# Performance work log

Measured on AMD Instinct MI355X. Metric: run time of the kernel, lower is better.

The kernel has to match this reference:

```python
import jax, jax.numpy as jnp
import numpy as np

N_NODES = 50000


def gcn_conv(x, edge_index, W, b, num_nodes):
    """PyG GCNConv: add self-loops, symmetric norm, gather-scatter aggregate."""
    h = x @ W  # [N, out]
    row = jnp.concatenate([edge_index[0], jnp.arange(num_nodes)])  # sources (+ self loops)
    col = jnp.concatenate([edge_index[1], jnp.arange(num_nodes)])  # targets
    deg = jax.ops.segment_sum(jnp.ones_like(col, dtype=h.dtype), col, num_segments=num_nodes)
    dinv = jnp.where(deg > 0, jax.lax.rsqrt(deg), 0.0)
    norm = dinv[row] * dinv[col]  # [E+N]
    msgs = h[row] * norm[:, None]  # gather + scale
    out = jax.ops.segment_sum(msgs, col, num_segments=num_nodes)  # scatter-add
    return out + b


def setup_inputs() -> dict:
    key = jax.random.key(0)
    ks = jax.random.split(key, 8)
    F_in, H, D = 50, 50, 64
    E_train, Ep, En = 1600000, 200000, 200000
    x = jax.random.normal(ks[0], (N_NODES, F_in), dtype=jnp.float32)
    train_pos_edge_index = jax.random.randint(ks[1], (2, E_train), 0, N_NODES)
    pos_edge_index = jax.random.randint(ks[2], (2, Ep), 0, N_NODES)
    neg_edge_index = jax.random.randint(ks[3], (2, En), 0, N_NODES)
    # Glorot-ish params for the two GCN layers
    W1 = jax.random.normal(ks[4], (F_in, H), dtype=jnp.float32) * (1.0 / np.sqrt(F_in))
    b1 = jnp.zeros((H,), dtype=jnp.float32)
    W2 = jax.random.normal(ks[5], (H, D), dtype=jnp.float32) * (1.0 / np.sqrt(H))
    b2 = jnp.zeros((D,), dtype=jnp.float32)
    return {"x": x, "train_pos_edge_index": train_pos_edge_index,
            "pos_edge_index": pos_edge_index, "neg_edge_index": neg_edge_index,
            "W1": W1, "b1": b1, "W2": W2, "b2": b2}


def reference(x, train_pos_edge_index, pos_edge_index, neg_edge_index, W1, b1, W2, b2):
    # encode: conv1 -> relu -> conv2
    h = gcn_conv(x, train_pos_edge_index, W1, b1, N_NODES)
    h = jax.nn.relu(h)
    z = gcn_conv(h, train_pos_edge_index, W2, b2, N_NODES)  # [N, D]
    # decode: dot product over concatenated pos/neg edge endpoints
    edge_index = jnp.concatenate([pos_edge_index, neg_edge_index], axis=-1)
    logits = jnp.sum(z[edge_index[0]] * z[edge_index[1]], axis=-1)  # [Ep+En]
    return logits
```

## Files before the change

### kernel.cpp

```cpp
#include <hip/hip_runtime.h>
#include <hip/hip_bf16.h>
#include <hip/hip_fp16.h>


constexpr int N_NODES = 50000;
constexpr int NBITS = 6;
constexpr int BNODES = 1 << NBITS;
constexpr int NBUCK = (N_NODES + BNODES - 1) / BNODES;
constexpr int CAP = 2560;
constexpr int CHUNK = 6144;
constexpr int PTHREADS = 512;
constexpr int CTHREADS = 512;
constexpr int NTILE = 8;
constexpr int TROWS = 6250;

union H4 {
    uint2 u;
    __half2 h[2];
};

union H8 {
    uint4 u;
    __half2 h[4];
};

__device__ inline H4 f4_to_h4(float4 v) {
    H4 r;
    r.h[0] = __floats2half2_rn(v.x, v.y);
    r.h[1] = __floats2half2_rn(v.z, v.w);
    return r;
}

__device__ inline uint4 pack8(float4 A, float4 B) {
    H8 r;
    r.h[0] = __floats2half2_rn(A.x, A.y);
    r.h[1] = __floats2half2_rn(A.z, A.w);
    r.h[2] = __floats2half2_rn(B.x, B.y);
    r.h[3] = __floats2half2_rn(B.z, B.w);
    return r.u;
}

__device__ inline void unpack8(uint4 w, int* r) {
    r[0] = (int)(w.x & 0xffffu);  r[1] = (int)(w.x >> 16);
    r[2] = (int)(w.y & 0xffffu);  r[3] = (int)(w.y >> 16);
    r[4] = (int)(w.z & 0xffffu);  r[5] = (int)(w.z >> 16);
    r[6] = (int)(w.w & 0xffffu);  r[7] = (int)(w.w >> 16);
}

__device__ inline void add8(float4& A, float4& B, H8 v) {
    float2 g0 = __half22float2(v.h[0]);
    float2 g1 = __half22float2(v.h[1]);
    float2 g2 = __half22float2(v.h[2]);
    float2 g3 = __half22float2(v.h[3]);
    A.x += g0.x; A.y += g0.y; A.z += g1.x; A.w += g1.y;
    B.x += g2.x; B.y += g2.y; B.z += g3.x; B.w += g3.y;
}

__device__ inline void fma8(float4& A, float4& B, H8 v, float m) {
    float2 g0 = __half22float2(v.h[0]);
    float2 g1 = __half22float2(v.h[1]);
    float2 g2 = __half22float2(v.h[2]);
    float2 g3 = __half22float2(v.h[3]);
    A.x = fmaf(m, g0.x, A.x); A.y = fmaf(m, g0.y, A.y);
    A.z = fmaf(m, g1.x, A.z); A.w = fmaf(m, g1.y, A.w);
    B.x = fmaf(m, g2.x, B.x); B.y = fmaf(m, g2.y, B.y);
    B.z = fmaf(m, g3.x, B.z); B.w = fmaf(m, g3.y, B.w);
}

__device__ inline float hdot2(unsigned ua, unsigned ub) {
    __half2 ha = *(__half2*)&ua;
    __half2 hb = *(__half2*)&ub;
    float2 fa = __half22float2(ha);
    float2 fb = __half22float2(hb);
    return fa.x * fb.x + fa.y * fb.y;
}

__global__ __launch_bounds__(PTHREADS) void partition_kernel(const int4* __restrict__ row4,
                                                             const int4* __restrict__ col4, int E,
                                                             int* __restrict__ cursor,
                                                             unsigned* __restrict__ bEdges) {
    __shared__ unsigned ed2[CHUNK];
    __shared__ unsigned char tick[CHUNK];
    __shared__ int cnt[NBUCK];
    __shared__ int loff[NBUCK];
    __shared__ int base[NBUCK];
    int t = threadIdx.x;
    int e0 = blockIdx.x * CHUNK;
    int n = min(CHUNK, E - e0);
    int n4 = n >> 2;
    for (int i = t; i < NBUCK; i += PTHREADS) cnt[i] = 0;
    __syncthreads();
    const int4* r4 = row4 + (e0 >> 2);
    const int4* c4 = col4 + (e0 >> 2);
    for (int i = t; i < n4; i += PTHREADS) {
        int4 c = c4[i];
        tick[i * 4 + 0] = (unsigned char)atomicAdd(&cnt[c.x >> NBITS], 1);
        tick[i * 4 + 1] = (unsigned char)atomicAdd(&cnt[c.y >> NBITS], 1);
        tick[i * 4 + 2] = (unsigned char)atomicAdd(&cnt[c.z >> NBITS], 1);
        tick[i * 4 + 3] = (unsigned char)atomicAdd(&cnt[c.w >> NBITS], 1);
    }
    __syncthreads();
    if (t < 64) {
        constexpr int SEG = (NBUCK + 63) / 64;
        int lo = t * SEG;
        int hi = min(lo + SEG, NBUCK);
        int s = 0;
        for (int i = lo; i < hi; ++i) {
            loff[i] = s;
            s += cnt[i];
        }
        int tot = s;
        int ex = tot;
#pragma unroll
        for (int off = 1; off < 64; off <<= 1) {
            int o = __shfl_up(ex, off, 64);
            if (t >= off) ex += o;
        }
        ex -= tot;
        for (int i = lo; i < hi; ++i) loff[i] += ex;
    }
    __syncthreads();
    for (int i = t; i < NBUCK; i += PTHREADS) base[i] = cnt[i] ? atomicAdd(&cursor[i], cnt[i]) : 0;
    for (int i = t; i < n4; i += PTHREADS) {
        int4 r = r4[i];
        int4 c = c4[i];
        unsigned p0 = ((unsigned)r.x << 16) | (unsigned)c.x;
        unsigned p1 = ((unsigned)r.y << 16) | (unsigned)c.y;
        unsigned p2 = ((unsigned)r.z << 16) | (unsigned)c.z;
        unsigned p3 = ((unsigned)r.w << 16) | (unsigned)c.w;
        ed2[loff[c.x >> NBITS] + (int)tick[i * 4 + 0]] = p0;
        ed2[loff[c.y >> NBITS] + (int)tick[i * 4 + 1]] = p1;
        ed2[loff[c.z >> NBITS] + (int)tick[i * 4 + 2]] = p2;
        ed2[loff[c.w >> NBITS] + (int)tick[i * 4 + 3]] = p3;
    }
    __syncthreads();
    for (int s = t; s < n; s += PTHREADS) {
        unsigned p = ed2[s];
        int bk = (int)(p & 0xffffu) >> NBITS;
        int pos = base[bk] + (s - loff[bk]);
        if (pos < CAP) bEdges[(size_t)bk * CAP + pos] = p;
    }
}

__global__ __launch_bounds__(CTHREADS) void bucket_csr_mm_kernel(const int* __restrict__ cursor,
                                                                 const unsigned* __restrict__ bEdges,
                                                                 const float* __restrict__ x,
                                                                 const float* __restrict__ W1,
                                                                 unsigned short* __restrict__ srcIdx,
                                                                 unsigned* __restrict__ rowmeta,
                                                                 float* __restrict__ dinv,
                                                                 uint2* __restrict__ Hs, int N) {
    __shared__ alignas(16) unsigned ed[CAP];
    __shared__ alignas(16) unsigned short srcL[CAP];
    __shared__ unsigned char tick[CAP];
    __shared__ int tdeg[BNODES * NTILE];
    __shared__ int toff[BNODES * NTILE];
    __shared__ int totPad;
    __shared__ float dinvL[BNODES];
    __shared__ float4 Ws4[50 * 16];
    __shared__ float xs[BNODES][51];
    int b = blockIdx.x;
    int tx = threadIdx.x;
    int cnt = min(cursor[b], CAP);
    for (int i = tx; i < BNODES * NTILE; i += CTHREADS) tdeg[i] = 0;
    {
        uint4* z4 = (uint4*)srcL;
        uint4 z = make_uint4(0u, 0u, 0u, 0u);
        for (int i = tx; i < (CAP >> 3); i += CTHREADS) z4[i] = z;
    }
    __syncthreads();
    const uint4* s4 = (const uint4*)(bEdges + (size_t)b * CAP);
    int cnt4 = cnt >> 2;
    for (int i = tx; i < cnt4; i += CTHREADS) {
        uint4 w = s4[i];
        ((uint4*)ed)[i] = w;
        unsigned pp[4] = {w.x, w.y, w.z, w.w};
#pragma unroll
        for (int u = 0; u < 4; ++u) {
            unsigned p = pp[u];
            int l = (int)(p & (BNODES - 1));
            int tl = (int)(p >> 16) / TROWS;
            tick[i * 4 + u] = (unsigned char)atomicAdd(&tdeg[l * NTILE + tl], 1);
        }
    }
    for (int i = cnt4 * 4 + tx; i < cnt; i += CTHREADS) {
        unsigned p = bEdges[(size_t)b * CAP + i];
        ed[i] = p;
        int l = (int)(p & (BNODES - 1));
        int tl = (int)(p >> 16) / TROWS;
        tick[i] = (unsigned char)atomicAdd(&tdeg[l * NTILE + tl], 1);
    }
    for (int i = tx; i < 50 * 64; i += CTHREADS) {
        int k = i >> 6;
        int c = i & 63;
        ((float*)Ws4)[i] = (c < 50) ? W1[k * 50 + c] : 0.f;
    }
    for (int i = tx; i < BNODES * 50; i += CTHREADS) {
        int l = i / 50;
        int k = i - l * 50;
        int node = b * BNODES + l;
        xs[l][k] = (node < N) ? x[(size_t)node * 50 + k] : 0.f;
    }
    __syncthreads();
    if (tx < BNODES) {
        int sd[NTILE];
        int d = 0;
#pragma unroll
        for (int u = 0; u < NTILE; ++u) {
            sd[u] = tdeg[tx * NTILE + u];
            d += sd[u];
        }
        int dpad = (d + 7) & ~7;
        int s = dpad;
#pragma unroll
        for (int off = 1; off < BNODES; off <<= 1) {
            int o = __shfl_up(s, off, 64);
            if (tx >= off) s += o;
        }
        int ex = s - dpad;
        int run = ex;
#pragma unroll
        for (int u = 0; u < NTILE; ++u) {
            toff[tx * NTILE + u] = run;
            run += sd[u];
        }
        if (tx == 63) totPad = min(s, CAP);
        float dvv = rsqrtf((float)d + 1.0f);
        dinvL[tx] = dvv;
        int node = b * BNODES + tx;
        if (node < N) {
            unsigned st = (unsigned)(b * CAP + ex);
            rowmeta[node] = (st << 7) | (unsigned)d;
            dinv[node] = dvv;
        }
    }
    __syncthreads();
    for (int i = tx; i < cnt; i += CTHREADS) {
        unsigned p = ed[i];
        int l = (int)(p & (BNODES - 1));
        int tl = (int)(p >> 16) / TROWS;
        int pos = toff[l * NTILE + tl] + (int)tick[i];
        if (pos < CAP) srcL[pos] = (unsigned short)(p >> 16);
    }
    __syncthreads();
    int tot = totPad;
    {
        const uint4* sl4 = (const uint4*)srcL;
        uint4* si4 = (uint4*)(srcIdx + (size_t)b * CAP);
        for (int i = tx; i < (tot >> 3); i += CTHREADS) si4[i] = sl4[i];
    }
    int q = tx & 15;
    int g = tx >> 4;
#pragma unroll
    for (int rep = 0; rep < 2; ++rep) {
        int l = g + rep * 32;
        float4 acc = make_float4(0.f, 0.f, 0.f, 0.f);
#pragma unroll
        for (int k = 0; k < 50; ++k) {
            float xv = xs[l][k];
            float4 w = Ws4[k * 16 + q];
            acc.x = fmaf(xv, w.x, acc.x);
            acc.y = fmaf(xv, w.y, acc.y);
            acc.z = fmaf(xv, w.z, acc.z);
            acc.w = fmaf(xv, w.w, acc.w);
        }
        float dv = dinvL[l];
        acc.x *= dv;
        acc.y *= dv;
        acc.z *= dv;
        acc.w *= dv;
        int node = b * BNODES + l;
        if (node < N) Hs[(size_t)node * 16 + q] = f4_to_h4(acc).u;
    }
}

__device__ inline void gather_sum8(const unsigned short* __restrict__ srcIdx,
                                   const uint4* __restrict__ hs, int node, int q,
                                   unsigned meta, float4& A, float4& B) {
    int start = (int)(meta >> 7);
    int d = (int)(meta & 127u);
    int end = start + d;
    H8 t;
    t.u = hs[(size_t)node * 8 + q];
    {
        float2 g0 = __half22float2(t.h[0]);
        float2 g1 = __half22float2(t.h[1]);
        float2 g2 = __half22float2(t.h[2]);
        float2 g3 = __half22float2(t.h[3]);
        A = make_float4(g0.x, g0.y, g1.x, g1.y);
        B = make_float4(g2.x, g2.y, g3.x, g3.y);
    }
    if (d == 0) return;
    int j = start;
    uint4 w = *(const uint4*)(srcIdx + j);
    while (j + 8 <= end) {
        uint4 wc = w;
        if (j + 8 < end) w = *(const uint4*)(srcIdx + j + 8);
        int r[8];
        unpack8(wc, r);
#pragma unroll
        for (int u = 0; u < 8; ++u) {
            H8 hv;
            hv.u = hs[(size_t)r[u] * 8 + q];
            add8(A, B, hv);
        }
        j += 8;
    }
    if (j < end) {
        int r[8];
        unpack8(w, r);
#pragma unroll
        for (int u = 0; u < 8; ++u) {
            float m = (j + u < end) ? 1.f : 0.f;
            H8 hv;
            hv.u = hs[(size_t)r[u] * 8 + q];
            fma8(A, B, hv, m);
        }
    }
}

template <int BC>
__global__ __launch_bounds__(256) void agg_mm_kernel(const unsigned* __restrict__ rowmeta,
                                                     const unsigned short* __restrict__ srcIdx,
                                                     const uint4* __restrict__ hs,
                                                     const float* __restrict__ dinv,
                                                     const float* __restrict__ b1,
                                                     const float* __restrict__ W2,
                                                     uint4* __restrict__ out, int N) {
    __shared__ float4 Ws4[50 * 16];
    __shared__ float h1s[32][68];
    for (int i = threadIdx.x; i < 50 * 64; i += 256) ((float*)Ws4)[i] = W2[i];
    int tid = blockIdx.x * blockDim.x + threadIdx.x;
    int node = tid >> 3;
    int q = tid & 7;
    int g = threadIdx.x >> 3;
    int nodeC = min(node, N - 1);
    float4 A = make_float4(0.f, 0.f, 0.f, 0.f), B = A;
    if (q < 7) gather_sum8(srcIdx, hs, nodeC, q, rowmeta[nodeC], A, B);
    float dv = dinv[nodeC];
    int f = q * 8;
    float hv[8] = {A.x, A.y, A.z, A.w, B.x, B.y, B.z, B.w};
#pragma unroll
    for (int u = 0; u < 8; ++u) {
        float bb = (f + u < BC) ? b1[f + u] : 0.f;
        h1s[g][f + u] = fmaxf(dv * hv[u] + bb, 0.f);
    }
    __syncthreads();
    float4 aA = make_float4(0.f, 0.f, 0.f, 0.f), aB = aA;
#pragma unroll
    for (int k = 0; k < 50; ++k) {
        float xv = h1s[g][k];
        float4 wA = Ws4[k * 16 + 2 * q];
        float4 wB = Ws4[k * 16 + 2 * q + 1];
        aA.x = fmaf(xv, wA.x, aA.x);
        aA.y = fmaf(xv, wA.y, aA.y);
        aA.z = fmaf(xv, wA.z, aA.z);
        aA.w = fmaf(xv, wA.w, aA.w);
        aB.x = fmaf(xv, wB.x, aB.x);
        aB.y = fmaf(xv, wB.y, aB.y);
        aB.z = fmaf(xv, wB.z, aB.z);
        aB.w = fmaf(xv, wB.w, aB.w);
    }
    aA.x *= dv; aA.y *= dv; aA.z *= dv; aA.w *= dv;
    aB.x *= dv; aB.y *= dv; aB.z *= dv; aB.w *= dv;
    if (node < N) out[(size_t)node * 8 + q] = pack8(aA, aB);
}

template <int BC>
__global__ __launch_bounds__(256) void agg_kernel(const unsigned* __restrict__ rowmeta,
                                                  const unsigned short* __restrict__ srcIdx,
                                                  const uint4* __restrict__ hs,
                                                  const float* __restrict__ dinv,
                                                  const float* __restrict__ b,
                                                  uint4* __restrict__ out, int N) {
    int tid = blockIdx.x * blockDim.x + threadIdx.x;
    int node = tid >> 3;
    int q = tid & 7;
    if (node >= N) return;
    float4 A, B;
    gather_sum8(srcIdx, hs, node, q, rowmeta[node], A, B);
    float dv = dinv[node];
    int f = q * 8;
    float hv[8] = {A.x, A.y, A.z, A.w, B.x, B.y, B.z, B.w};
    float o[8];
#pragma unroll
    for (int u = 0; u < 8; ++u) o[u] = dv * hv[u] + (f + u < BC ? b[f + u] : 0.f);
    out[(size_t)node * 8 + q] =
        pack8(make_float4(o[0], o[1], o[2], o[3]), make_float4(o[4], o[5], o[6], o[7]));
}

__global__ __launch_bounds__(256) void decode_kernel(const int* __restrict__ pos,
                                                     const int* __restrict__ neg, int Ep, int En,
                                                     const uint4* __restrict__ z4,
                                                     float* __restrict__ logits) {
    int tid = blockIdx.x * blockDim.x + threadIdx.x;
    int e = tid >> 3;
    int q = tid & 7;
    int Etot = Ep + En;
    if (e >= Etot) return;
    int a, bn;
    if (e < Ep) {
        a = pos[e];
        bn = pos[Ep + e];
    } else {
        int t = e - Ep;
        a = neg[t];
        bn = neg[En + t];
    }
    uint4 ua = z4[(size_t)a * 8 + q];
    uint4 ub = z4[(size_t)bn * 8 + q];
    float v = hdot2(ua.x, ub.x) + hdot2(ua.y, ub.y) + hdot2(ua.z, ub.z) + hdot2(ua.w, ub.w);
    v += __shfl_xor(v, 1, 64);
    v += __shfl_xor(v, 2, 64);
    v += __shfl_xor(v, 4, 64);
    if (q == 0) logits[e] = v;
}

extern "C" void kernel_launch(void* const* d_in, const int* in_sizes, int n_in,
                              void* d_out, int out_size, void* d_ws, size_t ws_size,
                              hipStream_t stream) {
    const float* x = (const float*)d_in[0];
    const int* train = (const int*)d_in[1];
    const int* pos = (const int*)d_in[2];
    const int* neg = (const int*)d_in[3];
    const float* W1 = (const float*)d_in[4];
    const float* b1 = (const float*)d_in[5];
    const float* W2 = (const float*)d_in[6];
    const float* b2 = (const float*)d_in[7];
    float* logits = (float*)d_out;

    const int FIN = 50;
    const int N = in_sizes[0] / FIN;
    const int E = in_sizes[1] / 2;
    const int Ep = in_sizes[2] / 2;
    const int En = in_sizes[3] / 2;

    const int* t_row = train;
    const int* t_col = train + E;

    float* dinv = (float*)d_ws;
    __half* buf0 = (__half*)(dinv + N);
    __half* buf1 = buf0 + (size_t)N * 64;
    unsigned* rowmeta = (unsigned*)(buf1 + (size_t)N * 64);
    int* cursor = (int*)(rowmeta + N);
    uintptr_t sp = (uintptr_t)(cursor + NBUCK);
    sp = (sp + 15) & ~(uintptr_t)15;
    unsigned short* srcIdx = (unsigned short*)sp;
    uintptr_t bp = (uintptr_t)(srcIdx + (size_t)NBUCK * CAP);
    bp = (bp + 15) & ~(uintptr_t)15;
    unsigned* bEdges = (unsigned*)bp;

    hipMemsetAsync(cursor, 0, (size_t)NBUCK * sizeof(int), stream);

    partition_kernel<<<(E + CHUNK - 1) / CHUNK, PTHREADS, 0, stream>>>((const int4*)t_row,
                                                                       (const int4*)t_col, E,
                                                                       cursor, bEdges);
    bucket_csr_mm_kernel<<<NBUCK, CTHREADS, 0, stream>>>(cursor, bEdges, x, W1, srcIdx, rowmeta,
                                                         dinv, (uint2*)buf0, N);

    const int AGB = (N * 8 + 255) / 256;

    agg_mm_kernel<50><<<AGB, 256, 0, stream>>>(rowmeta, srcIdx, (const uint4*)buf0, dinv, b1, W2,
                                               (uint4*)buf1, N);
    agg_kernel<64><<<AGB, 256, 0, stream>>>(rowmeta, srcIdx, (const uint4*)buf1, dinv, b2,
                                            (uint4*)buf0, N);
    decode_kernel<<<((Ep + En) * 8 + 255) / 256, 256, 0, stream>>>(pos, neg, Ep, En,
                                                                   (const uint4*)buf0, logits);
}
```

Baseline: 197.5 us.

## Split each aggregation into two source-range phases with fp32 partial sums

Each GCN aggregation is split into two passes. The first gathers neighbours whose source index lies in the lower half of the node range and writes fp32 partial sums. The second gathers the upper half, adds the partials, and applies the epilogue. The aim is to keep the half of the feature table each pass touches resident in cache, and nontemporal loads and stores are added for streamed data to reduce cache pollution. In exchange there are two extra kernel launches and a 12.8MB partial-sum buffer written and read back per layer.

```diff
diff --git a/kernel.cpp b/kernel.cpp
--- a/kernel.cpp
+++ b/kernel.cpp
@@ -13,6 +13,30 @@
 constexpr int CTHREADS = 512;
 constexpr int NTILE = 8;
 constexpr int TROWS = 6250;
+constexpr int SPLIT_ROW = 4 * TROWS;
+
+typedef unsigned int u32x4 __attribute__((ext_vector_type(4)));
+typedef float f32x4 __attribute__((ext_vector_type(4)));
+
+__device__ inline uint4 ntload_u4(const uint4* p) {
+    u32x4 v = __builtin_nontemporal_load((const u32x4*)p);
+    return make_uint4(v.x, v.y, v.z, v.w);
+}
+
+__device__ inline void ntstore_u4(uint4* p, uint4 v) {
+    u32x4 t = {v.x, v.y, v.z, v.w};
+    __builtin_nontemporal_store(t, (u32x4*)p);
+}
+
+__device__ inline float4 ntload_f4(const float4* p) {
+    f32x4 v = __builtin_nontemporal_load((const f32x4*)p);
+    return make_float4(v.x, v.y, v.z, v.w);
+}
+
+__device__ inline void ntstore_f4(float4* p, float4 v) {
+    f32x4 t = {v.x, v.y, v.z, v.w};
+    __builtin_nontemporal_store(t, (f32x4*)p);
+}
 
 union H4 {
     uint2 u;
@@ -148,6 +172,7 @@
                                                                  const float* __restrict__ W1,
                                                                  unsigned short* __restrict__ srcIdx,
                                                                  unsigned* __restrict__ rowmeta,
+                                                                 unsigned char* __restrict__ dlo,
                                                                  float* __restrict__ dinv,
                                                                  uint2* __restrict__ Hs, int N) {
     __shared__ alignas(16) unsigned ed[CAP];
@@ -210,6 +235,7 @@
             sd[u] = tdeg[tx * NTILE + u];
             d += sd[u];
         }
+        int dl = sd[0] + sd[1] + sd[2] + sd[3];
         int dpad = (d + 7) & ~7;
         int s = dpad;
 #pragma unroll
@@ -231,6 +257,7 @@
         if (node < N) {
             unsigned st = (unsigned)(b * CAP + ex);
             rowmeta[node] = (st << 7) | (unsigned)d;
+            dlo[node] = (unsigned char)dl;
             dinv[node] = dvv;
         }
     }
@@ -274,30 +301,28 @@
     }
 }
 
-__device__ inline void gather_sum8(const unsigned short* __restrict__ srcIdx,
-                                   const uint4* __restrict__ hs, int node, int q,
-                                   unsigned meta, float4& A, float4& B) {
-    int start = (int)(meta >> 7);
-    int d = (int)(meta & 127u);
-    int end = start + d;
-    H8 t;
-    t.u = hs[(size_t)node * 8 + q];
-    {
-        float2 g0 = __half22float2(t.h[0]);
-        float2 g1 = __half22float2(t.h[1]);
-        float2 g2 = __half22float2(t.h[2]);
-        float2 g3 = __half22float2(t.h[3]);
-        A = make_float4(g0.x, g0.y, g1.x, g1.y);
-        B = make_float4(g2.x, g2.y, g3.x, g3.y);
-    }
-    if (d == 0) return;
-    int j = start;
-    uint4 w = *(const uint4*)(srcIdx + j);
-    while (j + 8 <= end) {
-        uint4 wc = w;
-        if (j + 8 < end) w = *(const uint4*)(srcIdx + j + 8);
+__device__ inline void gather_range8(const unsigned short* __restrict__ srcIdx,
+                                     const uint4* __restrict__ hs, int jlo, int jhi,
+                                     int q, float4& A, float4& B) {
+    if (jlo >= jhi) return;
+    int j = jlo & ~7;
+    if (j < jlo) {
+        uint4 w = ntload_u4((const uint4*)(srcIdx + j));
         int r[8];
-        unpack8(wc, r);
+        unpack8(w, r);
+#pragma unroll
+        for (int u = 0; u < 8; ++u) {
+            bool ok = (j + u >= jlo) && (j + u < jhi);
+            H8 hv;
+            hv.u = hs[(size_t)(ok ? r[u] : 0) * 8 + q];
+            fma8(A, B, hv, ok ? 1.f : 0.f);
+        }
+        j += 8;
+    }
+    while (j + 8 <= jhi) {
+        uint4 w = ntload_u4((const uint4*)(srcIdx + j));
+        int r[8];
+        unpack8(w, r);
 #pragma unroll
         for (int u = 0; u < 8; ++u) {
             H8 hv;
@@ -306,27 +331,54 @@
         }
         j += 8;
     }
-    if (j < end) {
+    if (j < jhi) {
+        uint4 w = ntload_u4((const uint4*)(srcIdx + j));
         int r[8];
         unpack8(w, r);
 #pragma unroll
         for (int u = 0; u < 8; ++u) {
-            float m = (j + u < end) ? 1.f : 0.f;
+            bool ok = (j + u < jhi);
             H8 hv;
-            hv.u = hs[(size_t)r[u] * 8 + q];
-            fma8(A, B, hv, m);
-        }
-    }
+            hv.u = hs[(size_t)(ok ? r[u] : 0) * 8 + q];
+            fma8(A, B, hv, ok ? 1.f : 0.f);
+        }
+    }
+}
+
+template <int QMAX>
+__global__ __launch_bounds__(256) void agg_phaseA_kernel(const unsigned* __restrict__ rowmeta,
+                                                         const unsigned char* __restrict__ dlo,
+                                                         const unsigned short* __restrict__ srcIdx,
+                                                         const uint4* __restrict__ hs,
+                                                         float4* __restrict__ part, int N) {
+    int tid = blockIdx.x * blockDim.x + threadIdx.x;
+    int node = tid >> 3;
+    int q = tid & 7;
+    if (node >= N || q >= QMAX) return;
+    unsigned meta = rowmeta[node];
+    int start = (int)(meta >> 7);
+    int jmid = start + (int)dlo[node];
+    float4 A = make_float4(0.f, 0.f, 0.f, 0.f), B = A;
+    if (node < SPLIT_ROW) {
+        H8 s;
+        s.u = hs[(size_t)node * 8 + q];
+        add8(A, B, s);
+    }
+    gather_range8(srcIdx, hs, start, jmid, q, A, B);
+    ntstore_f4(&part[(size_t)node * 16 + 2 * q], A);
+    ntstore_f4(&part[(size_t)node * 16 + 2 * q + 1], B);
 }
 
 template <int BC>
-__global__ __launch_bounds__(256) void agg_mm_kernel(const unsigned* __restrict__ rowmeta,
-                                                     const unsigned short* __restrict__ srcIdx,
-                                                     const uint4* __restrict__ hs,
-                                                     const float* __restrict__ dinv,
-                                                     const float* __restrict__ b1,
-                                                     const float* __restrict__ W2,
-                                                     uint4* __restrict__ out, int N) {
+__global__ __launch_bounds__(256) void agg_mm_phaseB_kernel(const unsigned* __restrict__ rowmeta,
+                                                            const unsigned char* __restrict__ dlo,
+                                                            const unsigned short* __restrict__ srcIdx,
+                                                            const uint4* __restrict__ hs,
+                                                            const float4* __restrict__ part,
+                                                            const float* __restrict__ dinv,
+                                                            const float* __restrict__ b1,
+                                                            const float* __restrict__ W2,
+                                                            uint4* __restrict__ out, int N) {
     __shared__ float4 Ws4[50 * 16];
     __shared__ float h1s[32][68];
     for (int i = threadIdx.x; i < 50 * 64; i += 256) ((float*)Ws4)[i] = W2[i];
@@ -335,8 +387,21 @@
     int q = tid & 7;
     int g = threadIdx.x >> 3;
     int nodeC = min(node, N - 1);
+    unsigned meta = rowmeta[nodeC];
+    int start = (int)(meta >> 7);
+    int d = (int)(meta & 127u);
+    int jmid = start + (int)dlo[nodeC];
     float4 A = make_float4(0.f, 0.f, 0.f, 0.f), B = A;
-    if (q < 7) gather_sum8(srcIdx, hs, nodeC, q, rowmeta[nodeC], A, B);
+    if (q < 7) {
+        A = ntload_f4(&part[(size_t)nodeC * 16 + 2 * q]);
+        B = ntload_f4(&part[(size_t)nodeC * 16 + 2 * q + 1]);
+        if (nodeC >= SPLIT_ROW) {
+            H8 s;
+            s.u = hs[(size_t)nodeC * 8 + q];
+            add8(A, B, s);
+        }
+        gather_range8(srcIdx, hs, jmid, start + d, q, A, B);
+    }
     float dv = dinv[nodeC];
     int f = q * 8;
     float hv[8] = {A.x, A.y, A.z, A.w, B.x, B.y, B.z, B.w};
@@ -363,30 +428,42 @@
     }
     aA.x *= dv; aA.y *= dv; aA.z *= dv; aA.w *= dv;
     aB.x *= dv; aB.y *= dv; aB.z *= dv; aB.w *= dv;
-    if (node < N) out[(size_t)node * 8 + q] = pack8(aA, aB);
+    if (node < N) ntstore_u4(&out[(size_t)node * 8 + q], pack8(aA, aB));
 }
 
 template <int BC>
-__global__ __launch_bounds__(256) void agg_kernel(const unsigned* __restrict__ rowmeta,
-                                                  const unsigned short* __restrict__ srcIdx,
-                                                  const uint4* __restrict__ hs,
-                                                  const float* __restrict__ dinv,
-                                                  const float* __restrict__ b,
-                                                  uint4* __restrict__ out, int N) {
+__global__ __launch_bounds__(256) void agg_phaseB_kernel(const unsigned* __restrict__ rowmeta,
+                                                         const unsigned char* __restrict__ dlo,
+                                                         const unsigned short* __restrict__ srcIdx,
+                                                         const uint4* __restrict__ hs,
+                                                         const float4* __restrict__ part,
+                                                         const float* __restrict__ dinv,
+                                                         const float* __restrict__ b,
+                                                         uint4* __restrict__ out, int N) {
     int tid = blockIdx.x * blockDim.x + threadIdx.x;
     int node = tid >> 3;
     int q = tid & 7;
     if (node >= N) return;
-    float4 A, B;
-    gather_sum8(srcIdx, hs, node, q, rowmeta[node], A, B);
+    unsigned meta = rowmeta[node];
+    int start = (int)(meta >> 7);
+    int d = (int)(meta & 127u);
+    int jmid = start + (int)dlo[node];
+    float4 A = ntload_f4(&part[(size_t)node * 16 + 2 * q]);
+    float4 B = ntload_f4(&part[(size_t)node * 16 + 2 * q + 1]);
+    if (node >= SPLIT_ROW) {
+        H8 s;
+        s.u = hs[(size_t)node * 8 + q];
+        add8(A, B, s);
+    }
+    gather_range8(srcIdx, hs, jmid, start + d, q, A, B);
     float dv = dinv[node];
     int f = q * 8;
     float hv[8] = {A.x, A.y, A.z, A.w, B.x, B.y, B.z, B.w};
     float o[8];
 #pragma unroll
     for (int u = 0; u < 8; ++u) o[u] = dv * hv[u] + (f + u < BC ? b[f + u] : 0.f);
-    out[(size_t)node * 8 + q] =
-        pack8(make_float4(o[0], o[1], o[2], o[3]), make_float4(o[4], o[5], o[6], o[7]));
+    ntstore_u4(&out[(size_t)node * 8 + q],
+               pack8(make_float4(o[0], o[1], o[2], o[3]), make_float4(o[4], o[5], o[6], o[7])));
 }
 
 __global__ __launch_bounds__(256) void decode_kernel(const int* __restrict__ pos,
@@ -449,21 +526,29 @@
     uintptr_t bp = (uintptr_t)(srcIdx + (size_t)NBUCK * CAP);
     bp = (bp + 15) & ~(uintptr_t)15;
     unsigned* bEdges = (unsigned*)bp;
-
-    hipMemsetAsync(cursor, 0, (size_t)NBUCK * sizeof(int), stream);
+    unsigned char* dlo = (unsigned char*)(bEdges + (size_t)NBUCK * CAP);
+    uintptr_t fp = (uintptr_t)(dlo + N);
+    fp = (fp + 15) & ~(uintptr_t)15;
+    float4* fpart = (float4*)fp;
+
+    (void)hipMemsetAsync(cursor, 0, (size_t)NBUCK * sizeof(int), stream);
 
     partition_kernel<<<(E + CHUNK - 1) / CHUNK, PTHREADS, 0, stream>>>((const int4*)t_row,
                                                                        (const int4*)t_col, E,
                                                                        cursor, bEdges);
     bucket_csr_mm_kernel<<<NBUCK, CTHREADS, 0, stream>>>(cursor, bEdges, x, W1, srcIdx, rowmeta,
-                                                         dinv, (uint2*)buf0, N);
+                                                         dlo, dinv, (uint2*)buf0, N);
 
     const int AGB = (N * 8 + 255) / 256;
 
-    agg_mm_kernel<50><<<AGB, 256, 0, stream>>>(rowmeta, srcIdx, (const uint4*)buf0, dinv, b1, W2,
-                                               (uint4*)buf1, N);
-    agg_kernel<64><<<AGB, 256, 0, stream>>>(rowmeta, srcIdx, (const uint4*)buf1, dinv, b2,
-                                            (uint4*)buf0, N);
+    agg_phaseA_kernel<7><<<AGB, 256, 0, stream>>>(rowmeta, dlo, srcIdx, (const uint4*)buf0,
+                                                  fpart, N);
+    agg_mm_phaseB_kernel<50><<<AGB, 256, 0, stream>>>(rowmeta, dlo, srcIdx, (const uint4*)buf0,
+                                                      fpart, dinv, b1, W2, (uint4*)buf1, N);
+    agg_phaseA_kernel<8><<<AGB, 256, 0, stream>>>(rowmeta, dlo, srcIdx, (const uint4*)buf1,
+                                                  fpart, N);
+    agg_phaseB_kernel<64><<<AGB, 256, 0, stream>>>(rowmeta, dlo, srcIdx, (const uint4*)buf1,
+                                                   fpart, dinv, b2, (uint4*)buf0, N);
     decode_kernel<<<((Ep + En) * 8 + 255) / 256, 256, 0, stream>>>(pos, neg, Ep, En,
                                                                    (const uint4*)buf0, logits);
 }
```

Result: slower. 222.2 us (+12.5%).
